# Kernel optimization log

Hardware: AMD Instinct MI355X
Metric: run time of the kernel (lower is better)

Reference implementation:

```python
import jax, jax.numpy as jnp
import numpy as np

LAYER_NUMS = 3
# activations per layer: elu, elu, none (matches expert_activations=["elu","elu",null])
ACTS = [jax.nn.elu, jax.nn.elu, None]


def setup_inputs() -> dict:
    key = jax.random.key(0)
    k1, k2, k3, k4 = jax.random.split(key, 4)
    E, D, B_ = 8, 2048, 4096
    weight_blend = jax.random.uniform(k1, (E,), dtype=jnp.float32)
    x = jax.random.normal(k2, (B_, D), dtype=jnp.float32)
    W = jax.random.normal(k3, (LAYER_NUMS, E, D, D), dtype=jnp.float32) * 0.02
    B = jax.random.normal(k4, (LAYER_NUMS, D), dtype=jnp.float32) * 0.02
    return {"weight_blend": weight_blend, "x": x, "W": W, "B": B}


def reference(weight_blend, x, W, B):
    # Dropout is identity in eval/deterministic mode (expert_keep_prob=0.0).
    for i in range(LAYER_NUMS):
        # blended weight: sum_e c_e * W_e  -> (out, in)
        w = jnp.einsum("e,eoi->oi", weight_blend, W[i])
        x = x @ w.T + B[i]
        if ACTS[i] is not None:
            x = ACTS[i](x)
    return x
```

## Files before the change

kernel.cpp:

```cpp
#include <hip/hip_runtime.h>
#include <hip/hip_bf16.h>

#define MDIM 4096
#define NDIM 2048
#define KDIM 2048
#define KTILES 32

typedef __attribute__((ext_vector_type(8))) short bf16x8;
typedef __attribute__((ext_vector_type(4))) float f32x4;

__device__ __forceinline__ unsigned short f2bf(float f) {
    unsigned u = __builtin_bit_cast(unsigned, f);
    u += 0x7FFFu + ((u >> 16) & 1u);
    return (unsigned short)(u >> 16);
}

__global__ __launch_bounds__(256) void blend_convert_kernel(
    const float* __restrict__ W, const float* __restrict__ cb,
    const float* __restrict__ x,
    unsigned short* __restrict__ wb, unsigned short* __restrict__ xb)
{
    float c[8];
#pragma unroll
    for (int e = 0; e < 8; ++e) c[e] = cb[e];
    const unsigned per_layer = 4194304u;
    const unsigned wtotal4 = 3u * (per_layer >> 2);
    const unsigned xtotal4 = 2097152u;
    const unsigned total = wtotal4 + xtotal4;
    unsigned stride = gridDim.x * blockDim.x;
    for (unsigned i = blockIdx.x * blockDim.x + threadIdx.x; i < total; i += stride) {
        if (i < wtotal4) {
            unsigned layer = i >> 20;
            unsigned off = (i & 1048575u) << 2;
            const float* base = W + (size_t)layer * 8u * per_layer + off;
            float4 s = make_float4(0.f, 0.f, 0.f, 0.f);
#pragma unroll
            for (int e = 0; e < 8; ++e) {
                float4 v = *(const float4*)(base + (size_t)e * per_layer);
                s.x += c[e] * v.x; s.y += c[e] * v.y;
                s.z += c[e] * v.z; s.w += c[e] * v.w;
            }
            ushort4 o;
            o.x = f2bf(s.x); o.y = f2bf(s.y); o.z = f2bf(s.z); o.w = f2bf(s.w);
            *(ushort4*)(wb + (size_t)layer * per_layer + off) = o;
        } else {
            unsigned j = (i - wtotal4) << 2;
            float4 v = *(const float4*)(x + j);
            ushort4 o;
            o.x = f2bf(v.x); o.y = f2bf(v.y); o.z = f2bf(v.z); o.w = f2bf(v.w);
            *(ushort4*)(xb + j) = o;
        }
    }
}

#define BARR() do { asm volatile("" ::: "memory"); __builtin_amdgcn_s_barrier(); asm volatile("" ::: "memory"); } while (0)
#define SP(N) __builtin_amdgcn_s_setprio(N)
#define VMC(N) asm volatile("s_waitcnt vmcnt(" #N ")" ::: "memory")

template<int ACT, typename OutT>
__global__ __launch_bounds__(512, 2) void gemm_bn128(
    const unsigned short* __restrict__ A,
    const unsigned short* __restrict__ Bw,
    const float* __restrict__ bias,
    OutT* __restrict__ C)
{
    __shared__ __align__(16) unsigned short lds[73728];
    char* ldsc = (char*)lds;

    const int tid = threadIdx.x;
    const int wid = tid >> 6;
    const int lane = tid & 63;
    const int wr = wid >> 1;
    const int wc = wid & 1;

    const int wg = (blockIdx.x & 7) * 32 + (blockIdx.x >> 3);
    const size_t blockM = (size_t)(wg & 15) * 256;
    const size_t blockN = (size_t)(wg >> 4) * 128;

    const int sw = (lane & 7) << 4;
    const int ck = (lane >> 4) << 4;
    const int rAb = wr * 64 + (lane & 15);
    const int rBb = wc * 64 + (lane & 15);

    const int srow = tid >> 3;
    const int scol = ((tid & 7) ^ (srow & 7)) << 3;
    const unsigned short* aStage = A + (blockM + srow) * KDIM + scol;
    const unsigned short* bStage = Bw + (blockN + srow) * KDIM + scol;

#define STAGE_AS(BUF, S, KT) do { \
    const unsigned short* g_ = aStage + (size_t)(S) * 64 * KDIM + (size_t)(KT) * 64; \
    __builtin_amdgcn_global_load_lds((const __attribute__((address_space(1))) void*)g_, \
        (__attribute__((address_space(3))) void*)(ldsc + (BUF) * 49152 + (S) * 8192 + tid * 16), \
        16, 0, 0); \
} while (0)

#define STAGE_BS(BUF, S, KT) do { \
    const unsigned short* g_ = bStage + (size_t)(S) * 64 * KDIM + (size_t)(KT) * 64; \
    __builtin_amdgcn_global_load_lds((const __attribute__((address_space(1))) void*)g_, \
        (__attribute__((address_space(3))) void*)(ldsc + (BUF) * 49152 + 32768 + (S) * 8192 + tid * 16), \
        16, 0, 0); \
} while (0)

#define RD_A(BUF, M, KK) \
    (*(const bf16x8*)(ldsc + (BUF) * 49152 + ((rAb + (M) * 16)) * 128 + (((KK) * 64 + ck) ^ sw)))
#define RD_B(BUF, N, KK) \
    (*(const bf16x8*)(ldsc + (BUF) * 49152 + 32768 + (rBb + (N) * 16) * 128 + (((KK) * 64 + ck) ^ sw)))

    f32x4 acc[4][4];
#pragma unroll
    for (int m = 0; m < 4; ++m)
#pragma unroll
        for (int n = 0; n < 4; ++n) acc[m][n] = (f32x4){0.f, 0.f, 0.f, 0.f};

    STAGE_AS(0, 0, 0); STAGE_AS(0, 1, 0); STAGE_AS(0, 2, 0); STAGE_AS(0, 3, 0);
    STAGE_BS(0, 0, 0); STAGE_BS(0, 1, 0);
    STAGE_AS(1, 0, 1); STAGE_AS(1, 1, 1); STAGE_AS(1, 2, 1); STAGE_AS(1, 3, 1);
    STAGE_BS(1, 0, 1); STAGE_BS(1, 1, 1);
    VMC(6);
    BARR();

    int cur = 0;
#pragma unroll 1
    for (int t = 0; t < KTILES; ++t) {
        int stb = cur + 2; if (stb >= 3) stb -= 3;
        const int t1 = t + 1, t2 = t + 2;
        bf16x8 af[4][2], bf[4][2];
#pragma unroll
        for (int m = 0; m < 4; ++m) { af[m][0] = RD_A(cur, m, 0); af[m][1] = RD_A(cur, m, 1); }
#pragma unroll
        for (int n = 0; n < 4; ++n) { bf[n][0] = RD_B(cur, n, 0); bf[n][1] = RD_B(cur, n, 1); }
        if (t2 < KTILES) {
            STAGE_AS(stb, 0, t2); STAGE_AS(stb, 1, t2); STAGE_AS(stb, 2, t2); STAGE_AS(stb, 3, t2);
            STAGE_BS(stb, 0, t2); STAGE_BS(stb, 1, t2);
        }
        SP(1);
#pragma unroll
        for (int kk = 0; kk < 2; ++kk)
#pragma unroll
            for (int m = 0; m < 4; ++m)
#pragma unroll
                for (int n = 0; n < 4; ++n)
                    acc[m][n] = __builtin_amdgcn_mfma_f32_16x16x32_bf16(
                        af[m][kk], bf[n][kk], acc[m][n], 0, 0, 0);
        SP(0);
        if (t2 < KTILES) { VMC(6); }
        else if (t1 < KTILES) { VMC(0); }
        BARR();
        cur = cur + 1; if (cur >= 3) cur = 0;
    }

    const int crow = (lane >> 4) * 4;
    const int ccol = lane & 15;
#pragma unroll
    for (int m = 0; m < 4; ++m)
#pragma unroll
        for (int n = 0; n < 4; ++n) {
            const size_t col = blockN + wc * 64 + n * 16 + ccol;
            const float bv = bias[col];
#pragma unroll
            for (int r = 0; r < 4; ++r) {
                const size_t row = blockM + wr * 64 + m * 16 + crow + r;
                float v = acc[m][n][r] + bv;
                if (ACT) v = v > 0.f ? v : expm1f(v);
                if constexpr (sizeof(OutT) == 2) {
                    C[row * NDIM + col] = (OutT)f2bf(v);
                } else {
                    C[row * NDIM + col] = (OutT)v;
                }
            }
        }
#undef STAGE_AS
#undef STAGE_BS
#undef RD_A
#undef RD_B
}

extern "C" void kernel_launch(void* const* d_in, const int* in_sizes, int n_in,
                              void* d_out, int out_size, void* d_ws, size_t ws_size,
                              hipStream_t stream) {
    const float* blendw = (const float*)d_in[0];
    const float* x      = (const float*)d_in[1];
    const float* W      = (const float*)d_in[2];
    const float* Bb     = (const float*)d_in[3];
    float* out = (float*)d_out;

    unsigned short* wb = (unsigned short*)d_ws;
    unsigned short* xb = wb + (size_t)3 * 4194304;
    unsigned short* y0 = xb + 8388608;
    unsigned short* y1 = xb;

    blend_convert_kernel<<<2048, 256, 0, stream>>>(W, blendw, x, wb, xb);

    const int grid = (MDIM / 256) * (NDIM / 128);
    gemm_bn128<1, unsigned short><<<grid, 512, 0, stream>>>(xb, wb,               Bb,        y0);
    gemm_bn128<1, unsigned short><<<grid, 512, 0, stream>>>(y0, wb + 4194304,     Bb + 2048, y1);
    gemm_bn128<0, float        ><<<grid, 512, 0, stream>>>(y1, wb + 2 * 4194304,  Bb + 4096, out);
}
```

Before: 232.2 us.

## Load B operand directly from global into registers, stage only A in LDS

The GEMM no longer stages the weight (B) tile through LDS. Each wave loads its B fragments straight from global memory into registers, double-buffered across even and odd iterations, while A keeps a triple-buffered LDS pipeline. This shrinks LDS use and drops the LDS reads for B, aiming to relieve LDS bandwidth and allow more occupancy. The cost is duplicated global/L2 traffic for B across the wave rows, plus higher register pressure, and the B loads are less coalesced.

Result: slower. 382.7 us (+64.8%).

```diff
diff --git a/kernel.cpp b/kernel.cpp
--- a/kernel.cpp
+++ b/kernel.cpp
@@ -58,13 +58,13 @@
 #define VMC(N) asm volatile("s_waitcnt vmcnt(" #N ")" ::: "memory")
 
 template<int ACT, typename OutT>
-__global__ __launch_bounds__(512, 2) void gemm_bn128(
+__global__ __launch_bounds__(512, 2) void gemm_breg(
     const unsigned short* __restrict__ A,
     const unsigned short* __restrict__ Bw,
     const float* __restrict__ bias,
     OutT* __restrict__ C)
 {
-    __shared__ __align__(16) unsigned short lds[73728];
+    __shared__ __align__(16) unsigned short lds[49152];
     char* ldsc = (char*)lds;
 
     const int tid = threadIdx.x;
@@ -80,31 +80,37 @@
     const int sw = (lane & 7) << 4;
     const int ck = (lane >> 4) << 4;
     const int rAb = wr * 64 + (lane & 15);
-    const int rBb = wc * 64 + (lane & 15);
 
     const int srow = tid >> 3;
     const int scol = ((tid & 7) ^ (srow & 7)) << 3;
     const unsigned short* aStage = A + (blockM + srow) * KDIM + scol;
-    const unsigned short* bStage = Bw + (blockN + srow) * KDIM + scol;
-
-#define STAGE_AS(BUF, S, KT) do { \
-    const unsigned short* g_ = aStage + (size_t)(S) * 64 * KDIM + (size_t)(KT) * 64; \
-    __builtin_amdgcn_global_load_lds((const __attribute__((address_space(1))) void*)g_, \
-        (__attribute__((address_space(3))) void*)(ldsc + (BUF) * 49152 + (S) * 8192 + tid * 16), \
-        16, 0, 0); \
-} while (0)
-
-#define STAGE_BS(BUF, S, KT) do { \
-    const unsigned short* g_ = bStage + (size_t)(S) * 64 * KDIM + (size_t)(KT) * 64; \
-    __builtin_amdgcn_global_load_lds((const __attribute__((address_space(1))) void*)g_, \
-        (__attribute__((address_space(3))) void*)(ldsc + (BUF) * 49152 + 32768 + (S) * 8192 + tid * 16), \
-        16, 0, 0); \
-} while (0)
+
+    const unsigned short* bPtr =
+        Bw + (size_t)(blockN + wc * 64 + (lane & 15)) * KDIM + ((lane >> 4) * 8);
+
+#define STAGE_A4(BUF, KT) do { \
+    _Pragma("unroll") for (int s_ = 0; s_ < 4; ++s_) { \
+        const unsigned short* g_ = aStage + (size_t)s_ * 64 * KDIM + (size_t)(KT) * 64; \
+        __builtin_amdgcn_global_load_lds((const __attribute__((address_space(1))) void*)g_, \
+            (__attribute__((address_space(3))) void*)(ldsc + (BUF) * 32768 + s_ * 8192 + tid * 16), \
+            16, 0, 0); \
+    } } while (0)
 
 #define RD_A(BUF, M, KK) \
-    (*(const bf16x8*)(ldsc + (BUF) * 49152 + ((rAb + (M) * 16)) * 128 + (((KK) * 64 + ck) ^ sw)))
-#define RD_B(BUF, N, KK) \
-    (*(const bf16x8*)(ldsc + (BUF) * 49152 + 32768 + (rBb + (N) * 16) * 128 + (((KK) * 64 + ck) ^ sw)))
+    (*(const bf16x8*)(ldsc + (BUF) * 32768 + (rAb + (M) * 16) * 128 + (((KK) * 64 + ck) ^ sw)))
+
+#define READ_A(BUF) do { _Pragma("unroll") for (int m_ = 0; m_ < 4; ++m_) { \
+    af[m_][0] = RD_A(BUF, m_, 0); af[m_][1] = RD_A(BUF, m_, 1); } } while (0)
+
+#define LOAD_B(DST, T) do { _Pragma("unroll") for (int n_ = 0; n_ < 4; ++n_) { \
+    DST[n_][0] = *(const bf16x8*)(bPtr + (size_t)(n_ * 16) * KDIM + (size_t)(T) * 64); \
+    DST[n_][1] = *(const bf16x8*)(bPtr + (size_t)(n_ * 16) * KDIM + (size_t)(T) * 64 + 32); } } while (0)
+
+#define DO_MFMA(BREG) do { _Pragma("unroll") for (int kk_ = 0; kk_ < 2; ++kk_) \
+    _Pragma("unroll") for (int m_ = 0; m_ < 4; ++m_) \
+    _Pragma("unroll") for (int n_ = 0; n_ < 4; ++n_) \
+        acc[m_][n_] = __builtin_amdgcn_mfma_f32_16x16x32_bf16( \
+            af[m_][kk_], BREG[n_][kk_], acc[m_][n_], 0, 0, 0); } while (0)
 
     f32x4 acc[4][4];
 #pragma unroll
@@ -112,41 +118,36 @@
 #pragma unroll
         for (int n = 0; n < 4; ++n) acc[m][n] = (f32x4){0.f, 0.f, 0.f, 0.f};
 
-    STAGE_AS(0, 0, 0); STAGE_AS(0, 1, 0); STAGE_AS(0, 2, 0); STAGE_AS(0, 3, 0);
-    STAGE_BS(0, 0, 0); STAGE_BS(0, 1, 0);
-    STAGE_AS(1, 0, 1); STAGE_AS(1, 1, 1); STAGE_AS(1, 2, 1); STAGE_AS(1, 3, 1);
-    STAGE_BS(1, 0, 1); STAGE_BS(1, 1, 1);
-    VMC(6);
+    bf16x8 af[4][2], bE[4][2], bO[4][2];
+
+    STAGE_A4(0, 0);
+    LOAD_B(bE, 0);
+    STAGE_A4(1, 1);
+    VMC(4);
     BARR();
 
-    int cur = 0;
+    int c0 = 0, c1 = 1, c2 = 2;
 #pragma unroll 1
-    for (int t = 0; t < KTILES; ++t) {
-        int stb = cur + 2; if (stb >= 3) stb -= 3;
-        const int t1 = t + 1, t2 = t + 2;
-        bf16x8 af[4][2], bf[4][2];
-#pragma unroll
-        for (int m = 0; m < 4; ++m) { af[m][0] = RD_A(cur, m, 0); af[m][1] = RD_A(cur, m, 1); }
-#pragma unroll
-        for (int n = 0; n < 4; ++n) { bf[n][0] = RD_B(cur, n, 0); bf[n][1] = RD_B(cur, n, 1); }
-        if (t2 < KTILES) {
-            STAGE_AS(stb, 0, t2); STAGE_AS(stb, 1, t2); STAGE_AS(stb, 2, t2); STAGE_AS(stb, 3, t2);
-            STAGE_BS(stb, 0, t2); STAGE_BS(stb, 1, t2);
-        }
-        SP(1);
-#pragma unroll
-        for (int kk = 0; kk < 2; ++kk)
-#pragma unroll
-            for (int m = 0; m < 4; ++m)
-#pragma unroll
-                for (int n = 0; n < 4; ++n)
-                    acc[m][n] = __builtin_amdgcn_mfma_f32_16x16x32_bf16(
-                        af[m][kk], bf[n][kk], acc[m][n], 0, 0, 0);
-        SP(0);
-        if (t2 < KTILES) { VMC(6); }
-        else if (t1 < KTILES) { VMC(0); }
-        BARR();
-        cur = cur + 1; if (cur >= 3) cur = 0;
+    for (int t = 0; t < KTILES; t += 2) {
+        {
+            const int u = t;
+            READ_A(c0);
+            if (u + 1 < KTILES) LOAD_B(bO, u + 1);
+            if (u + 2 < KTILES) STAGE_A4(c2, u + 2);
+            SP(1); DO_MFMA(bE); SP(0);
+            if (u < KTILES - 2) { VMC(4); } else { VMC(0); }
+            BARR();
+        }
+        {
+            const int u = t + 1;
+            READ_A(c1);
+            if (u + 1 < KTILES) LOAD_B(bE, u + 1);
+            if (u + 2 < KTILES) STAGE_A4(c0, u + 2);
+            SP(1); DO_MFMA(bO); SP(0);
+            if (u < KTILES - 2) { VMC(4); } else { VMC(0); }
+            BARR();
+        }
+        int tmp = c0; c0 = c2; c2 = c1; c1 = tmp;
     }
 
     const int crow = (lane >> 4) * 4;
@@ -169,10 +170,11 @@
                 }
             }
         }
-#undef STAGE_AS
-#undef STAGE_BS
+#undef STAGE_A4
 #undef RD_A
-#undef RD_B
+#undef READ_A
+#undef LOAD_B
+#undef DO_MFMA
 }
 
 extern "C" void kernel_launch(void* const* d_in, const int* in_sizes, int n_in,
@@ -192,7 +194,7 @@
     blend_convert_kernel<<<2048, 256, 0, stream>>>(W, blendw, x, wb, xb);
 
     const int grid = (MDIM / 256) * (NDIM / 128);
-    gemm_bn128<1, unsigned short><<<grid, 512, 0, stream>>>(xb, wb,               Bb,        y0);
-    gemm_bn128<1, unsigned short><<<grid, 512, 0, stream>>>(y0, wb + 4194304,     Bb + 2048, y1);
-    gemm_bn128<0, float        ><<<grid, 512, 0, stream>>>(y1, wb + 2 * 4194304,  Bb + 4096, out);
-}
+    gemm_breg<1, unsigned short><<<grid, 512, 0, stream>>>(xb, wb,               Bb,        y0);
+    gemm_breg<1, unsigned short><<<grid, 512, 0, stream>>>(y0, wb + 4194304,     Bb + 2048, y1);
+    gemm_breg<0, float        ><<<grid, 512, 0, stream>>>(y1, wb + 2 * 4194304,  Bb + 4096, out);
+}
```

## Overlap next-layer weight blending with current GEMM main loop

Applied to the files above, without the earlier changes.

The up-front kernel now blends only layer 0's weights (plus the x conversion). Each GEMM blends and converts the next layer's weights, interleaved with its own K-loop in 8 chunks, so that memory-bound blending overlaps MFMA compute. The cost is extra global loads and registers inside the GEMM. The blend loads also lengthen the vmcnt accounting (VMC(15)), which could stall the software pipeline or lower occupancy.

New measurement: 204.8 us. 11.8% less time.

```diff
diff --git a/kernel.cpp b/kernel.cpp
--- a/kernel.cpp
+++ b/kernel.cpp
@@ -5,6 +5,7 @@
 #define NDIM 2048
 #define KDIM 2048
 #define KTILES 32
+#define PER_LAYER 4194304
 
 typedef __attribute__((ext_vector_type(8))) short bf16x8;
 typedef __attribute__((ext_vector_type(4))) float f32x4;
@@ -15,7 +16,7 @@
     return (unsigned short)(u >> 16);
 }
 
-__global__ __launch_bounds__(256) void blend_convert_kernel(
+__global__ __launch_bounds__(256) void blend0_kernel(
     const float* __restrict__ W, const float* __restrict__ cb,
     const float* __restrict__ x,
     unsigned short* __restrict__ wb, unsigned short* __restrict__ xb)
@@ -23,26 +24,24 @@
     float c[8];
 #pragma unroll
     for (int e = 0; e < 8; ++e) c[e] = cb[e];
-    const unsigned per_layer = 4194304u;
-    const unsigned wtotal4 = 3u * (per_layer >> 2);
+    const unsigned wtotal4 = PER_LAYER >> 2;
     const unsigned xtotal4 = 2097152u;
     const unsigned total = wtotal4 + xtotal4;
     unsigned stride = gridDim.x * blockDim.x;
     for (unsigned i = blockIdx.x * blockDim.x + threadIdx.x; i < total; i += stride) {
         if (i < wtotal4) {
-            unsigned layer = i >> 20;
-            unsigned off = (i & 1048575u) << 2;
-            const float* base = W + (size_t)layer * 8u * per_layer + off;
+            unsigned off = i << 2;
+            const float* base = W + off;
             float4 s = make_float4(0.f, 0.f, 0.f, 0.f);
 #pragma unroll
             for (int e = 0; e < 8; ++e) {
-                float4 v = *(const float4*)(base + (size_t)e * per_layer);
+                float4 v = *(const float4*)(base + (size_t)e * PER_LAYER);
                 s.x += c[e] * v.x; s.y += c[e] * v.y;
                 s.z += c[e] * v.z; s.w += c[e] * v.w;
             }
             ushort4 o;
             o.x = f2bf(s.x); o.y = f2bf(s.y); o.z = f2bf(s.z); o.w = f2bf(s.w);
-            *(ushort4*)(wb + (size_t)layer * per_layer + off) = o;
+            *(ushort4*)(wb + off) = o;
         } else {
             unsigned j = (i - wtotal4) << 2;
             float4 v = *(const float4*)(x + j);
@@ -55,14 +54,18 @@
 
 #define BARR() do { asm volatile("" ::: "memory"); __builtin_amdgcn_s_barrier(); asm volatile("" ::: "memory"); } while (0)
 #define SP(N) __builtin_amdgcn_s_setprio(N)
-#define VMC(N) asm volatile("s_waitcnt vmcnt(" #N ")" ::: "memory")
-
-template<int ACT, typename OutT>
-__global__ __launch_bounds__(512, 2) void gemm_bn128(
+#define VMC_IMPL(N) asm volatile("s_waitcnt vmcnt(" #N ")" ::: "memory")
+#define VMC(N) VMC_IMPL(N)
+
+template<int ACT, typename OutT, int BLEND>
+__global__ __launch_bounds__(512, 2) void gemm_fused(
     const unsigned short* __restrict__ A,
     const unsigned short* __restrict__ Bw,
     const float* __restrict__ bias,
-    OutT* __restrict__ C)
+    OutT* __restrict__ C,
+    const float* __restrict__ Wnext,
+    const float* __restrict__ cb,
+    unsigned short* __restrict__ wbNext)
 {
     __shared__ __align__(16) unsigned short lds[73728];
     char* ldsc = (char*)lds;
@@ -73,6 +76,13 @@
     const int wr = wid >> 1;
     const int wc = wid & 1;
 
+    float cw[8];
+    if (BLEND) {
+#pragma unroll
+        for (int e = 0; e < 8; ++e) cw[e] = cb[e];
+        VMC(0);
+    }
+
     const int wg = (blockIdx.x & 7) * 32 + (blockIdx.x >> 3);
     const size_t blockM = (size_t)(wg & 15) * 256;
     const size_t blockN = (size_t)(wg >> 4) * 128;
@@ -111,6 +121,44 @@
     for (int m = 0; m < 4; ++m)
 #pragma unroll
         for (int n = 0; n < 4; ++n) acc[m][n] = (f32x4){0.f, 0.f, 0.f, 0.f};
+
+#define GEMM_ITER(T, WAITER) do { \
+    int stb_ = cur + 2; if (stb_ >= 3) stb_ -= 3; \
+    bf16x8 af[4][2], bfr[4][2]; \
+    _Pragma("unroll") for (int m_ = 0; m_ < 4; ++m_) { \
+        af[m_][0] = RD_A(cur, m_, 0); af[m_][1] = RD_A(cur, m_, 1); } \
+    _Pragma("unroll") for (int n_ = 0; n_ < 4; ++n_) { \
+        bfr[n_][0] = RD_B(cur, n_, 0); bfr[n_][1] = RD_B(cur, n_, 1); } \
+    if ((T) + 2 < KTILES) { \
+        STAGE_AS(stb_, 0, (T) + 2); STAGE_AS(stb_, 1, (T) + 2); \
+        STAGE_AS(stb_, 2, (T) + 2); STAGE_AS(stb_, 3, (T) + 2); \
+        STAGE_BS(stb_, 0, (T) + 2); STAGE_BS(stb_, 1, (T) + 2); \
+    } \
+    SP(1); \
+    _Pragma("unroll") for (int kk_ = 0; kk_ < 2; ++kk_) \
+    _Pragma("unroll") for (int m_ = 0; m_ < 4; ++m_) \
+    _Pragma("unroll") for (int n_ = 0; n_ < 4; ++n_) \
+        acc[m_][n_] = __builtin_amdgcn_mfma_f32_16x16x32_bf16( \
+            af[m_][kk_], bfr[n_][kk_], acc[m_][n_], 0, 0, 0); \
+    SP(0); \
+    WAITER; \
+    BARR(); \
+    cur = cur + 1; if (cur >= 3) cur = 0; \
+} while (0)
+
+#define BLEND_STEP(G) do { \
+    const unsigned idx_ = (unsigned)(G) * 131072u + (unsigned)blockIdx.x * 512u + (unsigned)tid; \
+    const unsigned off_ = idx_ << 2; \
+    const float* bs_ = Wnext + off_; \
+    float4 s_ = make_float4(0.f, 0.f, 0.f, 0.f); \
+    _Pragma("unroll") for (int e_ = 0; e_ < 8; ++e_) { \
+        float4 v_ = *(const float4*)(bs_ + (size_t)e_ * PER_LAYER); \
+        s_.x += cw[e_] * v_.x; s_.y += cw[e_] * v_.y; \
+        s_.z += cw[e_] * v_.z; s_.w += cw[e_] * v_.w; } \
+    ushort4 o_; \
+    o_.x = f2bf(s_.x); o_.y = f2bf(s_.y); o_.z = f2bf(s_.z); o_.w = f2bf(s_.w); \
+    *(ushort4*)(wbNext + off_) = o_; \
+} while (0)
 
     STAGE_AS(0, 0, 0); STAGE_AS(0, 1, 0); STAGE_AS(0, 2, 0); STAGE_AS(0, 3, 0);
     STAGE_BS(0, 0, 0); STAGE_BS(0, 1, 0);
@@ -120,34 +168,23 @@
     BARR();
 
     int cur = 0;
+    if (BLEND) {
 #pragma unroll 1
-    for (int t = 0; t < KTILES; ++t) {
-        int stb = cur + 2; if (stb >= 3) stb -= 3;
-        const int t1 = t + 1, t2 = t + 2;
-        bf16x8 af[4][2], bf[4][2];
-#pragma unroll
-        for (int m = 0; m < 4; ++m) { af[m][0] = RD_A(cur, m, 0); af[m][1] = RD_A(cur, m, 1); }
-#pragma unroll
-        for (int n = 0; n < 4; ++n) { bf[n][0] = RD_B(cur, n, 0); bf[n][1] = RD_B(cur, n, 1); }
-        if (t2 < KTILES) {
-            STAGE_AS(stb, 0, t2); STAGE_AS(stb, 1, t2); STAGE_AS(stb, 2, t2); STAGE_AS(stb, 3, t2);
-            STAGE_BS(stb, 0, t2); STAGE_BS(stb, 1, t2);
+        for (int g = 0; g < 8; ++g) {
+            const int t0 = 3 * g;
+            GEMM_ITER(t0, VMC(6));
+            BLEND_STEP(g);
+            GEMM_ITER(t0 + 1, VMC(15));
+            GEMM_ITER(t0 + 2, VMC(6));
         }
-        SP(1);
-#pragma unroll
-        for (int kk = 0; kk < 2; ++kk)
-#pragma unroll
-            for (int m = 0; m < 4; ++m)
-#pragma unroll
-                for (int n = 0; n < 4; ++n)
-                    acc[m][n] = __builtin_amdgcn_mfma_f32_16x16x32_bf16(
-                        af[m][kk], bf[n][kk], acc[m][n], 0, 0, 0);
-        SP(0);
-        if (t2 < KTILES) { VMC(6); }
-        else if (t1 < KTILES) { VMC(0); }
-        BARR();
-        cur = cur + 1; if (cur >= 3) cur = 0;
+#pragma unroll 1
+        for (int t = 24; t < 30; ++t) GEMM_ITER(t, VMC(6));
+    } else {
+#pragma unroll 1
+        for (int t = 0; t < 30; ++t) GEMM_ITER(t, VMC(6));
     }
+    GEMM_ITER(30, VMC(0));
+    GEMM_ITER(31, VMC(0));
 
     const int crow = (lane >> 4) * 4;
     const int ccol = lane & 15;
@@ -173,6 +210,8 @@
 #undef STAGE_BS
 #undef RD_A
 #undef RD_B
+#undef GEMM_ITER
+#undef BLEND_STEP
 }
 
 extern "C" void kernel_launch(void* const* d_in, const int* in_sizes, int n_in,
@@ -184,15 +223,19 @@
     const float* Bb     = (const float*)d_in[3];
     float* out = (float*)d_out;
 
-    unsigned short* wb = (unsigned short*)d_ws;
-    unsigned short* xb = wb + (size_t)3 * 4194304;
-    unsigned short* y0 = xb + 8388608;
-    unsigned short* y1 = xb;
-
-    blend_convert_kernel<<<2048, 256, 0, stream>>>(W, blendw, x, wb, xb);
-
-    const int grid = (MDIM / 256) * (NDIM / 128);
-    gemm_bn128<1, unsigned short><<<grid, 512, 0, stream>>>(xb, wb,               Bb,        y0);
-    gemm_bn128<1, unsigned short><<<grid, 512, 0, stream>>>(y0, wb + 4194304,     Bb + 2048, y1);
-    gemm_bn128<0, float        ><<<grid, 512, 0, stream>>>(y1, wb + 2 * 4194304,  Bb + 4096, out);
-}
+    unsigned short* wb0 = (unsigned short*)d_ws;
+    unsigned short* wb1 = wb0 + PER_LAYER;
+    unsigned short* wb2 = wb1 + PER_LAYER;
+    unsigned short* xb  = wb2 + PER_LAYER;
+    unsigned short* y0  = xb + 8388608;
+    unsigned short* y1  = xb;
+
+    blend0_kernel<<<2048, 256, 0, stream>>>(W, blendw, x, wb0, xb);
+
+    gemm_fused<1, unsigned short, 1><<<256, 512, 0, stream>>>(
+        xb, wb0, Bb,        y0,  W + (size_t)8 * PER_LAYER,  blendw, wb1);
+    gemm_fused<1, unsigned short, 1><<<256, 512, 0, stream>>>(
+        y0, wb1, Bb + 2048, y1,  W + (size_t)16 * PER_LAYER, blendw, wb2);
+    gemm_fused<0, float, 0><<<256, 512, 0, stream>>>(
+        y1, wb2, Bb + 4096, out, nullptr, nullptr, nullptr);
+}
```
